# Kernel tuning notes

Hardware: AMD Instinct MI355X
Metric: run time of the kernel (lower is better)

## Reference

```python
import jax, jax.numpy as jnp
import numpy as np

SEQ_LEN, BATCH, INPUT_SIZE, HIDDEN_SIZE = 2048, 64, 512, 512


def _xavier_uniform(key, shape, dtype=jnp.float32):
    fan_out, fan_in = shape
    limit = float(np.sqrt(6.0 / (fan_in + fan_out)))
    return jax.random.uniform(key, shape, dtype, -limit, limit)


def setup_inputs() -> dict:
    key = jax.random.key(0)
    kx, kh, kW, kU, kb1, kb2 = jax.random.split(key, 6)
    x = jax.random.normal(kx, (SEQ_LEN, BATCH, INPUT_SIZE), dtype=jnp.float32)
    prev_hidden = jax.random.normal(kh, (BATCH, HIDDEN_SIZE), dtype=jnp.float32)
    W = _xavier_uniform(kW, (HIDDEN_SIZE, INPUT_SIZE))
    U = _xavier_uniform(kU, (HIDDEN_SIZE, HIDDEN_SIZE))
    # torch nn.init.uniform_ default is U(0, 1)
    hidden_bias = jax.random.uniform(kb1, (HIDDEN_SIZE,), dtype=jnp.float32)
    input_bias = jax.random.uniform(kb2, (HIDDEN_SIZE,), dtype=jnp.float32)
    return {"x": x, "prev_hidden": prev_hidden, "W": W, "U": U,
            "hidden_bias": hidden_bias, "input_bias": input_bias}


def reference(x, prev_hidden, W, U, hidden_bias, input_bias):
    # Faithful to the source: the loop never updates `prev_hidden`, so the
    # recurrent term U @ h0 + b_h is CONSTANT across timesteps and each
    # output is out_t = tanh(W x_t + b_in + U h0 + b_h). This vectorizes
    # into one batched GEMM over all timesteps plus a broadcast add.
    # x: (T, B, I); W: (H, I); U: (H, H)
    wx = jnp.einsum('tbi,hi->tbh', x, W) + input_bias          # (T, B, H)
    uh = prev_hidden @ U.T + hidden_bias                        # (B, H)
    outputs = jnp.tanh(wx + uh[None, :, :])                     # (T, B, H)
    hidden = outputs[-1]                                        # (B, H)
    return outputs, hidden
```

## Files before the change

### kernel.cpp

```cpp
#include <hip/hip_runtime.h>
#include <hip/hip_bf16.h>
#include <cstdint>
#include <cstddef>


#define T_LEN 2048
#define BATCH 64
#define ISZ 512
#define HSZ 512
#define MTOT (T_LEN * BATCH)

#define BM 128
#define BN 128
#define BK 64

typedef __attribute__((ext_vector_type(8))) __bf16 bf16x8;
typedef __attribute__((ext_vector_type(4))) __bf16 bf16x4;
typedef __attribute__((ext_vector_type(4))) float f32x4;

#define GLOBAL_AS __attribute__((address_space(1)))
#define LDS_AS __attribute__((address_space(3)))

__device__ __forceinline__ float fast_tanh(float v) {
    float e = __expf(2.0f * v);
    return 1.0f - 2.0f / (e + 1.0f);
}

__global__ __launch_bounds__(256) void convw_kernel(const float* __restrict__ W,
                                                    __bf16* __restrict__ Wbf) {
    int i = blockIdx.x * 256 + threadIdx.x;
    f32x4 f = ((const f32x4*)W)[i];
    bf16x4 v;
    v[0] = (__bf16)f[0]; v[1] = (__bf16)f[1];
    v[2] = (__bf16)f[2]; v[3] = (__bf16)f[3];
    ((bf16x4*)Wbf)[i] = v;
}

__global__ __launch_bounds__(512) void uh_kernel(const float* __restrict__ prev,
                                                 const float* __restrict__ U,
                                                 const float* __restrict__ hb,
                                                 const float* __restrict__ ib,
                                                 float* __restrict__ uh) {
    __shared__ float sp[HSZ];
    int b = blockIdx.x, h = threadIdx.x;
    sp[h] = prev[b * HSZ + h];
    __syncthreads();
    const float* urow = U + (size_t)h * HSZ;
    float acc = 0.f;
#pragma unroll 4
    for (int i = 0; i < HSZ; i += 4) {
        f32x4 u4 = *(const f32x4*)(urow + i);
        acc += u4[0] * sp[i] + u4[1] * sp[i + 1] + u4[2] * sp[i + 2] + u4[3] * sp[i + 3];
    }
    uh[b * HSZ + h] = acc + hb[h] + ib[h];
}

__global__ __launch_bounds__(256, 2) void gemm_tanh_kernel(
        const float* __restrict__ x, const __bf16* __restrict__ Wbf,
        const float* __restrict__ uh, float* __restrict__ out) {
    __shared__ __attribute__((aligned(16))) __bf16 sA[BM * BK];
    __shared__ __attribute__((aligned(16))) __bf16 sB[BN * BK];

    int orig = blockIdx.x;
    int wg = (orig & 7) * 512 + (orig >> 3);
    int mt = wg >> 2, nt = wg & 3;

    int tid = threadIdx.x;
    int lane = tid & 63, wid = tid >> 6;
    int wr = wid >> 1, wc = wid & 1;
    int l15 = lane & 15, l4 = lane >> 4;

    f32x4 acc[4][4] = {};

    const size_t m0 = (size_t)mt * BM;
    const int n0 = nt * BN;

#pragma unroll 1
    for (int ks = 0; ks < ISZ; ks += BK) {
#pragma unroll
        for (int it = 0; it < 4; ++it) {
            int p = it * 256 + tid;
            int row = p >> 3, pc = p & 7;
            const float* src = x + (m0 + row) * ISZ + ks + pc * 8;
            f32x4 f0 = *(const f32x4*)src;
            f32x4 f1 = *(const f32x4*)(src + 4);
            bf16x8 v;
            v[0] = (__bf16)f0[0]; v[1] = (__bf16)f0[1];
            v[2] = (__bf16)f0[2]; v[3] = (__bf16)f0[3];
            v[4] = (__bf16)f1[0]; v[5] = (__bf16)f1[1];
            v[6] = (__bf16)f1[2]; v[7] = (__bf16)f1[3];
            *(bf16x8*)&sA[row * BK + pc * 8] = v;
        }
#pragma unroll
        for (int j = 0; j < 4; ++j) {
            int chunk = wid * 4 + j;
            int o = chunk * 1024 + lane * 16;
            int n = o >> 7;
            int c = (o & 127) >> 1;
            const __bf16* g = Wbf + (size_t)(n0 + n) * ISZ + ks + c;
            __builtin_amdgcn_global_load_lds((const GLOBAL_AS uint32_t*)g,
                                             (LDS_AS uint32_t*)((char*)sB + chunk * 1024),
                                             16, 0, 0);
        }
        __syncthreads();
#pragma unroll
        for (int kk = 0; kk < 2; ++kk) {
            bf16x8 af[4], bfr[4];
#pragma unroll
            for (int mi = 0; mi < 4; ++mi)
                af[mi] = *(const bf16x8*)&sA[(wr * 64 + mi * 16 + l15) * BK + kk * 32 + l4 * 8];
#pragma unroll
            for (int ni = 0; ni < 4; ++ni)
                bfr[ni] = *(const bf16x8*)&sB[(wc * 64 + ni * 16 + l15) * BK + kk * 32 + l4 * 8];
#pragma unroll
            for (int mi = 0; mi < 4; ++mi)
#pragma unroll
                for (int ni = 0; ni < 4; ++ni)
                    acc[mi][ni] = __builtin_amdgcn_mfma_f32_16x16x32_bf16(
                        af[mi], bfr[ni], acc[mi][ni], 0, 0, 0);
        }
        __syncthreads();
    }

#pragma unroll
    for (int mi = 0; mi < 4; ++mi) {
#pragma unroll
        for (int ni = 0; ni < 4; ++ni) {
#pragma unroll
            for (int r = 0; r < 4; ++r) {
                int ml = wr * 64 + mi * 16 + l4 * 4 + r;
                size_t m = m0 + ml;
                int n = n0 + wc * 64 + ni * 16 + l15;
                float v = acc[mi][ni][r] + uh[(ml & 63) * HSZ + n];
                out[m * HSZ + n] = fast_tanh(v);
            }
        }
    }
}

__global__ __launch_bounds__(256) void copyh_kernel(const float* __restrict__ out,
                                                    float* __restrict__ hid) {
    int i = blockIdx.x * 256 + threadIdx.x;
    hid[i] = out[(size_t)(MTOT - BATCH) * HSZ + i];
}

extern "C" void kernel_launch(void* const* d_in, const int* in_sizes, int n_in,
                              void* d_out, int out_size, void* d_ws, size_t ws_size,
                              hipStream_t stream) {
    const float* x  = (const float*)d_in[0];
    const float* ph = (const float*)d_in[1];
    const float* W  = (const float*)d_in[2];
    const float* U  = (const float*)d_in[3];
    const float* hb = (const float*)d_in[4];
    const float* ib = (const float*)d_in[5];
    float* out = (float*)d_out;

    __bf16* Wbf = (__bf16*)d_ws;
    float* uh   = (float*)((char*)d_ws + 512 * 1024);

    hipLaunchKernelGGL(convw_kernel, dim3(256), dim3(256), 0, stream, W, Wbf);
    hipLaunchKernelGGL(uh_kernel, dim3(64), dim3(512), 0, stream, ph, U, hb, ib, uh);
    hipLaunchKernelGGL(gemm_tanh_kernel, dim3(4096), dim3(256), 0, stream, x, Wbf, uh, out);
    hipLaunchKernelGGL(copyh_kernel, dim3(128), dim3(256), 0, stream,
                       out, out + (size_t)MTOT * HSZ);
}
```

Baseline: 232.1 us.

## Double-buffer GEMM tiles with XOR-swizzled LDS, vectorized epilogue, fuse hidden copy

The GEMM kernel now double-buffers the A and B tiles in shared memory. The next K-slice is loaded from global memory into registers and LDS while the current slice is being multiplied, which hides load latency behind MFMA work. Both LDS tiles use an XOR swizzle on 16-byte chunks to reduce bank conflicts. Swapping the MFMA operands transposes the accumulator layout, so the epilogue can load uh and write the output as float4 vectors, and the final hidden-state copy is folded into the last tile, removing one kernel launch. The cost is twice the LDS and the loss of the 2-blocks-per-SM launch bound hint, which may lower occupancy.

```diff
diff --git a/kernel.cpp b/kernel.cpp
--- a/kernel.cpp
+++ b/kernel.cpp
@@ -13,6 +13,7 @@
 #define BM 128
 #define BN 128
 #define BK 64
+#define NMT (MTOT / BM)
 
 typedef __attribute__((ext_vector_type(8))) __bf16 bf16x8;
 typedef __attribute__((ext_vector_type(4))) __bf16 bf16x4;
@@ -55,11 +56,12 @@
     uh[b * HSZ + h] = acc + hb[h] + ib[h];
 }
 
-__global__ __launch_bounds__(256, 2) void gemm_tanh_kernel(
+__global__ __launch_bounds__(256) void gemm_tanh_kernel(
         const float* __restrict__ x, const __bf16* __restrict__ Wbf,
-        const float* __restrict__ uh, float* __restrict__ out) {
-    __shared__ __attribute__((aligned(16))) __bf16 sA[BM * BK];
-    __shared__ __attribute__((aligned(16))) __bf16 sB[BN * BK];
+        const float* __restrict__ uh, float* __restrict__ out,
+        float* __restrict__ hid) {
+    __shared__ __attribute__((aligned(16))) __bf16 sA[2][BM * BK];
+    __shared__ __attribute__((aligned(16))) __bf16 sB[2][BN * BK];
 
     int orig = blockIdx.x;
     int wg = (orig & 7) * 512 + (orig >> 3);
@@ -70,78 +72,108 @@
     int wr = wid >> 1, wc = wid & 1;
     int l15 = lane & 15, l4 = lane >> 4;
 
-    f32x4 acc[4][4] = {};
-
     const size_t m0 = (size_t)mt * BM;
     const int n0 = nt * BN;
 
-#pragma unroll 1
-    for (int ks = 0; ks < ISZ; ks += BK) {
+    f32x4 acc[4][4] = {};
+    f32x4 aPre[8];
+
+    auto stageB = [&](int buf, int ks) {
+#pragma unroll
+        for (int j = 0; j < 4; ++j) {
+            int chunk = wid * 4 + j;
+            int row = chunk * 8 + (lane >> 3);
+            int cb = ((lane & 7) ^ (lane >> 3)) << 4;
+            const __bf16* g = Wbf + (size_t)(n0 + row) * ISZ + ks + (cb >> 1);
+            __builtin_amdgcn_global_load_lds((const GLOBAL_AS uint32_t*)g,
+                (LDS_AS uint32_t*)((char*)sB[buf] + chunk * 1024), 16, 0, 0);
+        }
+    };
+    auto loadA = [&](int ks) {
 #pragma unroll
         for (int it = 0; it < 4; ++it) {
             int p = it * 256 + tid;
             int row = p >> 3, pc = p & 7;
             const float* src = x + (m0 + row) * ISZ + ks + pc * 8;
-            f32x4 f0 = *(const f32x4*)src;
-            f32x4 f1 = *(const f32x4*)(src + 4);
+            aPre[2 * it]     = *(const f32x4*)src;
+            aPre[2 * it + 1] = *(const f32x4*)(src + 4);
+        }
+    };
+    auto writeA = [&](int buf) {
+#pragma unroll
+        for (int it = 0; it < 4; ++it) {
+            int p = it * 256 + tid;
+            int row = p >> 3, pc = p & 7;
+            f32x4 f0 = aPre[2 * it], f1 = aPre[2 * it + 1];
             bf16x8 v;
             v[0] = (__bf16)f0[0]; v[1] = (__bf16)f0[1];
             v[2] = (__bf16)f0[2]; v[3] = (__bf16)f0[3];
             v[4] = (__bf16)f1[0]; v[5] = (__bf16)f1[1];
             v[6] = (__bf16)f1[2]; v[7] = (__bf16)f1[3];
-            *(bf16x8*)&sA[row * BK + pc * 8] = v;
+            int cb = (pc * 16) ^ ((row & 7) << 4);
+            *(bf16x8*)((char*)sA[buf] + row * 128 + cb) = v;
         }
-#pragma unroll
-        for (int j = 0; j < 4; ++j) {
-            int chunk = wid * 4 + j;
-            int o = chunk * 1024 + lane * 16;
-            int n = o >> 7;
-            int c = (o & 127) >> 1;
-            const __bf16* g = Wbf + (size_t)(n0 + n) * ISZ + ks + c;
-            __builtin_amdgcn_global_load_lds((const GLOBAL_AS uint32_t*)g,
-                                             (LDS_AS uint32_t*)((char*)sB + chunk * 1024),
-                                             16, 0, 0);
-        }
-        __syncthreads();
+    };
+    auto compute = [&](int buf) {
 #pragma unroll
         for (int kk = 0; kk < 2; ++kk) {
             bf16x8 af[4], bfr[4];
 #pragma unroll
-            for (int mi = 0; mi < 4; ++mi)
-                af[mi] = *(const bf16x8*)&sA[(wr * 64 + mi * 16 + l15) * BK + kk * 32 + l4 * 8];
+            for (int mi = 0; mi < 4; ++mi) {
+                int row = wr * 64 + mi * 16 + l15;
+                int cb = (kk * 64 + l4 * 16) ^ ((row & 7) << 4);
+                af[mi] = *(const bf16x8*)((const char*)sA[buf] + row * 128 + cb);
+            }
 #pragma unroll
-            for (int ni = 0; ni < 4; ++ni)
-                bfr[ni] = *(const bf16x8*)&sB[(wc * 64 + ni * 16 + l15) * BK + kk * 32 + l4 * 8];
+            for (int ni = 0; ni < 4; ++ni) {
+                int row = wc * 64 + ni * 16 + l15;
+                int cb = (kk * 64 + l4 * 16) ^ ((row & 7) << 4);
+                bfr[ni] = *(const bf16x8*)((const char*)sB[buf] + row * 128 + cb);
+            }
 #pragma unroll
             for (int mi = 0; mi < 4; ++mi)
 #pragma unroll
                 for (int ni = 0; ni < 4; ++ni)
                     acc[mi][ni] = __builtin_amdgcn_mfma_f32_16x16x32_bf16(
-                        af[mi], bfr[ni], acc[mi][ni], 0, 0, 0);
+                        bfr[ni], af[mi], acc[mi][ni], 0, 0, 0);
         }
+    };
+
+    stageB(0, 0);
+    loadA(0);
+    writeA(0);
+    __syncthreads();
+
+#pragma unroll 2
+    for (int t = 0; t < 7; ++t) {
+        int cur = t & 1, nxt = cur ^ 1;
+        int ks = (t + 1) * BK;
+        loadA(ks);
+        stageB(nxt, ks);
+        compute(cur);
+        writeA(nxt);
         __syncthreads();
     }
+    compute(1);
 
+    bool lastTile = (mt == NMT - 1);
 #pragma unroll
     for (int mi = 0; mi < 4; ++mi) {
+        int ml = wr * 64 + mi * 16 + l15;
+        size_t m = m0 + ml;
+        int bb = ml & 63;
 #pragma unroll
         for (int ni = 0; ni < 4; ++ni) {
+            int nb = n0 + wc * 64 + ni * 16 + l4 * 4;
+            f32x4 u4 = *(const f32x4*)&uh[bb * HSZ + nb];
+            f32x4 v;
 #pragma unroll
-            for (int r = 0; r < 4; ++r) {
-                int ml = wr * 64 + mi * 16 + l4 * 4 + r;
-                size_t m = m0 + ml;
-                int n = n0 + wc * 64 + ni * 16 + l15;
-                float v = acc[mi][ni][r] + uh[(ml & 63) * HSZ + n];
-                out[m * HSZ + n] = fast_tanh(v);
-            }
+            for (int r = 0; r < 4; ++r) v[r] = fast_tanh(acc[mi][ni][r] + u4[r]);
+            *(f32x4*)&out[m * HSZ + nb] = v;
+            if (lastTile && ml >= BM - BATCH)
+                *(f32x4*)&hid[(size_t)(ml - (BM - BATCH)) * HSZ + nb] = v;
         }
     }
-}
-
-__global__ __launch_bounds__(256) void copyh_kernel(const float* __restrict__ out,
-                                                    float* __restrict__ hid) {
-    int i = blockIdx.x * 256 + threadIdx.x;
-    hid[i] = out[(size_t)(MTOT - BATCH) * HSZ + i];
 }
 
 extern "C" void kernel_launch(void* const* d_in, const int* in_sizes, int n_in,
@@ -154,13 +186,13 @@
     const float* hb = (const float*)d_in[4];
     const float* ib = (const float*)d_in[5];
     float* out = (float*)d_out;
+    float* hid = out + (size_t)MTOT * HSZ;
 
     __bf16* Wbf = (__bf16*)d_ws;
     float* uh   = (float*)((char*)d_ws + 512 * 1024);
 
     hipLaunchKernelGGL(convw_kernel, dim3(256), dim3(256), 0, stream, W, Wbf);
     hipLaunchKernelGGL(uh_kernel, dim3(64), dim3(512), 0, stream, ph, U, hb, ib, uh);
-    hipLaunchKernelGGL(gemm_tanh_kernel, dim3(4096), dim3(256), 0, stream, x, Wbf, uh, out);
-    hipLaunchKernelGGL(copyh_kernel, dim3(128), dim3(256), 0, stream,
-                       out, out + (size_t)MTOT * HSZ);
+    hipLaunchKernelGGL(gemm_tanh_kernel, dim3(4096), dim3(256), 0, stream,
+                       x, Wbf, uh, out, hid);
 }
```

Measured after the change: 266.1 us. 14.7% more time.
